# Performance work log

Hardware: AMD Instinct MI355X
Metric: run time of the kernel (lower is better)

## Reference

```python
import jax, jax.numpy as jnp
import numpy as np

PHI = (1.0 + 5.0 ** 0.5) / 2.0  # golden ratio used by the 'GenesisGeometry' engine
NUM_NODES, DIM = 65536, 512


def setup_inputs() -> dict:
    key = jax.random.key(0)
    state = jax.random.normal(key, (NUM_NODES, DIM), dtype=jnp.float32) * 0.01
    return {"state": state}


def _fuse_fields(x, left_v, right_v):
    # golden-ratio-weighted fusion of self + ring neighbors
    return (PHI * x + left_v + right_v) / (PHI + 2.0)


def _engine(fused):
    # GenesisGeometry: five correlated nonlinear outputs in one pass
    t = jnp.tanh(fused)
    bloom = jnp.tanh(PHI * fused)
    identity_next = fused + (1.0 / PHI) * t          # contractive state update
    crown = jax.nn.sigmoid(PHI * fused)
    triad = jnp.sin(fused) * jnp.cos(PHI * fused)
    spiral = fused * jnp.exp(-jnp.abs(fused) / PHI)
    return bloom, identity_next, crown, triad, spiral


def reference(state):
    # ring neighbor gather: x[(i-1)%N] == roll(+1), x[(i+1)%N] == roll(-1)
    left_v = jnp.roll(state, 1, axis=0)
    right_v = jnp.roll(state, -1, axis=0)
    fused = _fuse_fields(state, left_v, right_v)
    bloom, identity_next, crown, triad, spiral = _engine(fused)
    # stack outputs: (5, num_nodes, dim) -> [state, bloom, crown, triad, spiral]
    return jnp.stack([identity_next, bloom, crown, triad, spiral], axis=0)
```

## Files before the change

### kernel.cpp

```cpp
#include <hip/hip_runtime.h>
#include <math.h>


#define NUM_NODES 65536
#define DIM 512

typedef float f32x4 __attribute__((ext_vector_type(4)));

__global__ __launch_bounds__(256) void genesis_kernel(
    const f32x4* __restrict__ x, f32x4* __restrict__ out, int tot4) {
  const float phi      = 1.61803398874989484820f;
  const float inv_phi  = 0.61803398874989484820f;
  const float inv_p2   = 1.0f / (phi + 2.0f);
  const int row4 = DIM / 4;

  int stride = gridDim.x * blockDim.x;
  for (int e = blockIdx.x * blockDim.x + threadIdx.x; e < tot4; e += stride) {
    int l = e - row4; if (l < 0)     l += tot4;
    int r = e + row4; if (r >= tot4) r -= tot4;

    f32x4 c = x[e];
    f32x4 lv = x[l];
    f32x4 rv = x[r];

    f32x4 v_id, v_bl, v_cr, v_tr, v_sp;
#pragma unroll
    for (int j = 0; j < 4; ++j) {
      float f = (phi * c[j] + lv[j] + rv[j]) * inv_p2;

      float e2 = __expf(2.0f * f);
      float t = (e2 - 1.0f) * __builtin_amdgcn_rcpf(e2 + 1.0f);

      float ep = __expf(phi * f);
      float ep2 = ep * ep;
      float bloom = (ep2 - 1.0f) * __builtin_amdgcn_rcpf(ep2 + 1.0f);
      float crown = ep * __builtin_amdgcn_rcpf(ep + 1.0f);

      v_id[j] = f + inv_phi * t;
      v_bl[j] = bloom;
      v_cr[j] = crown;
      v_tr[j] = __sinf(f) * __cosf(phi * f);
      v_sp[j] = f * __expf(-fabsf(f) * inv_phi);
    }

    __builtin_nontemporal_store(v_id, &out[0 * (size_t)tot4 + e]);
    __builtin_nontemporal_store(v_bl, &out[1 * (size_t)tot4 + e]);
    __builtin_nontemporal_store(v_cr, &out[2 * (size_t)tot4 + e]);
    __builtin_nontemporal_store(v_tr, &out[3 * (size_t)tot4 + e]);
    __builtin_nontemporal_store(v_sp, &out[4 * (size_t)tot4 + e]);
  }
}

extern "C" void kernel_launch(void* const* d_in, const int* in_sizes, int n_in,
                              void* d_out, int out_size, void* d_ws, size_t ws_size,
                              hipStream_t stream) {
  const f32x4* x = (const f32x4*)d_in[0];
  f32x4* out = (f32x4*)d_out;
  int tot4 = in_sizes[0] / 4;

  const int block = 256;
  const int grid = 2048;
  genesis_kernel<<<grid, block, 0, stream>>>(x, out, tot4);
}
```

Measured before the change: 141.7 us.

## Process four rows per thread and reuse neighbor rows from registers

Each thread now handles four consecutive rows of one column vector. It loads six rows (a halo of one row on each side) into registers and reuses them across the stencil, so each input element is read 1.5 times instead of 3 times. The grid-stride loop is replaced by a fixed grid of N_ROWS/8 blocks with sizes hardcoded. Memory-level parallelism changes, and the output writes, which dominate traffic, stay the same.

```diff
diff --git a/kernel.cpp b/kernel.cpp
--- a/kernel.cpp
+++ b/kernel.cpp
@@ -2,52 +2,63 @@
 #include <math.h>
 
 
-#define NUM_NODES 65536
-#define DIM 512
+#define N_ROWS 65536
+#define COLS4 128
 
 typedef float f32x4 __attribute__((ext_vector_type(4)));
 
 __global__ __launch_bounds__(256) void genesis_kernel(
-    const f32x4* __restrict__ x, f32x4* __restrict__ out, int tot4) {
-  const float phi      = 1.61803398874989484820f;
-  const float inv_phi  = 0.61803398874989484820f;
-  const float inv_p2   = 1.0f / (phi + 2.0f);
-  const int row4 = DIM / 4;
+    const f32x4* __restrict__ x, f32x4* __restrict__ out) {
+  const float phi     = 1.61803398874989484820f;
+  const float inv_phi = 0.61803398874989484820f;
+  const float inv_p2  = 1.0f / (phi + 2.0f);
 
-  int stride = gridDim.x * blockDim.x;
-  for (int e = blockIdx.x * blockDim.x + threadIdx.x; e < tot4; e += stride) {
-    int l = e - row4; if (l < 0)     l += tot4;
-    int r = e + row4; if (r >= tot4) r -= tot4;
+  const int t = threadIdx.x;
+  const int c = t & 127;
+  const int rsub = t >> 7;
+  const int r0 = blockIdx.x * 8 + rsub * 4;
 
-    f32x4 c = x[e];
-    f32x4 lv = x[l];
-    f32x4 rv = x[r];
+  int rm = r0 - 1; if (rm < 0) rm += N_ROWS;
+  int rp = r0 + 4; if (rp >= N_ROWS) rp -= N_ROWS;
 
+  f32x4 L0 = x[(size_t)rm * COLS4 + c];
+  f32x4 L1 = x[(size_t)(r0 + 0) * COLS4 + c];
+  f32x4 L2 = x[(size_t)(r0 + 1) * COLS4 + c];
+  f32x4 L3 = x[(size_t)(r0 + 2) * COLS4 + c];
+  f32x4 L4 = x[(size_t)(r0 + 3) * COLS4 + c];
+  f32x4 L5 = x[(size_t)rp * COLS4 + c];
+  f32x4 L[6] = {L0, L1, L2, L3, L4, L5};
+
+  const size_t plane = (size_t)N_ROWS * COLS4;
+
+#pragma unroll
+  for (int k = 0; k < 4; ++k) {
+    size_t o = (size_t)(r0 + k) * COLS4 + c;
     f32x4 v_id, v_bl, v_cr, v_tr, v_sp;
 #pragma unroll
     for (int j = 0; j < 4; ++j) {
-      float f = (phi * c[j] + lv[j] + rv[j]) * inv_p2;
+      float f = (phi * L[k + 1][j] + L[k][j] + L[k + 2][j]) * inv_p2;
 
       float e2 = __expf(2.0f * f);
-      float t = (e2 - 1.0f) * __builtin_amdgcn_rcpf(e2 + 1.0f);
+      float tnh = (e2 - 1.0f) * __builtin_amdgcn_rcpf(e2 + 1.0f);
 
       float ep = __expf(phi * f);
       float ep2 = ep * ep;
       float bloom = (ep2 - 1.0f) * __builtin_amdgcn_rcpf(ep2 + 1.0f);
       float crown = ep * __builtin_amdgcn_rcpf(ep + 1.0f);
 
-      v_id[j] = f + inv_phi * t;
+      v_id[j] = f + inv_phi * tnh;
       v_bl[j] = bloom;
       v_cr[j] = crown;
       v_tr[j] = __sinf(f) * __cosf(phi * f);
       v_sp[j] = f * __expf(-fabsf(f) * inv_phi);
     }
 
-    __builtin_nontemporal_store(v_id, &out[0 * (size_t)tot4 + e]);
-    __builtin_nontemporal_store(v_bl, &out[1 * (size_t)tot4 + e]);
-    __builtin_nontemporal_store(v_cr, &out[2 * (size_t)tot4 + e]);
-    __builtin_nontemporal_store(v_tr, &out[3 * (size_t)tot4 + e]);
-    __builtin_nontemporal_store(v_sp, &out[4 * (size_t)tot4 + e]);
+    __builtin_nontemporal_store(v_id, &out[0 * plane + o]);
+    __builtin_nontemporal_store(v_bl, &out[1 * plane + o]);
+    __builtin_nontemporal_store(v_cr, &out[2 * plane + o]);
+    __builtin_nontemporal_store(v_tr, &out[3 * plane + o]);
+    __builtin_nontemporal_store(v_sp, &out[4 * plane + o]);
   }
 }
 
@@ -56,9 +67,8 @@
                               hipStream_t stream) {
   const f32x4* x = (const f32x4*)d_in[0];
   f32x4* out = (f32x4*)d_out;
-  int tot4 = in_sizes[0] / 4;
 
   const int block = 256;
-  const int grid = 2048;
-  genesis_kernel<<<grid, block, 0, stream>>>(x, out, tot4);
+  const int grid = N_ROWS / 8;
+  genesis_kernel<<<grid, block, 0, stream>>>(x, out);
 }
```

New measurement: 130.8 us. -7.6%, faster.
